# Kernel tuning notes

Measured on AMD Instinct MI355X. Metric: run time of the kernel, lower is better.

## Reference

```python
import jax, jax.numpy as jnp
import numpy as np

IN_FEATURES = 4096
OUT_FEATURES = 4096

def setup_inputs() -> dict:
    key = jax.random.key(0)
    kx, kw, kb = jax.random.split(key, 3)
    x = jax.random.normal(kx, (8192, IN_FEATURES), dtype=jnp.float32)
    weight = jax.random.normal(kw, (OUT_FEATURES, IN_FEATURES), dtype=jnp.float32)
    bias = jax.random.normal(kb, (OUT_FEATURES,), dtype=jnp.float32)
    return {"x": x, "weight": weight, "bias": bias}

def reference(x, weight, bias):
    # Binarize weights to {-1, 0, +1} via sign, then dense linear: y = x @ sign(W)^T + b
    w_bin = jnp.sign(weight)
    return jnp.einsum('bi,oi->bo', x, w_bin) + bias
```

## Files before the change

kernel.cpp:

```cpp
#include <hip/hip_runtime.h>
#include <hip/hip_bf16.h>
#include <stdint.h>

#define M_DIM 8192
#define N_DIM 4096
#define K_DIM 4096

#define NT 64

using i32x4 = __attribute__((ext_vector_type(4))) int;

typedef const __attribute__((address_space(1))) void glb_void_t;
typedef __attribute__((address_space(3))) void lds_void_t;

__device__ __forceinline__ void async16(const void* g, void* l) {
    __builtin_amdgcn_global_load_lds((glb_void_t*)(uintptr_t)g,
                                     (lds_void_t*)(uint32_t)(uintptr_t)l,
                                     16, 0, 0);
}

__device__ __forceinline__ int sgn_i8(float f) {
    union { float f; uint32_t u; } v; v.f = f;
    if ((v.u & 0x7FFFFFFFu) == 0u) return 0;
    return (v.u >> 31) ? -1 : 1;
}


__global__ void convert_w_kernel(const float* __restrict__ w,
                                 unsigned char* __restrict__ wq, int n4) {
    int stride = gridDim.x * blockDim.x;
    for (int i = blockIdx.x * blockDim.x + threadIdx.x; i < n4; i += stride) {
        float4 v = ((const float4*)w)[i];
        uint32_t o = ((uint32_t)(uint8_t)sgn_i8(v.x)) |
                     ((uint32_t)(uint8_t)sgn_i8(v.y) << 8) |
                     ((uint32_t)(uint8_t)sgn_i8(v.z) << 16) |
                     ((uint32_t)(uint8_t)sgn_i8(v.w) << 24);
        ((uint32_t*)wq)[i] = o;
    }
}


__global__ __launch_bounds__(256)
void convert_x_kernel(const float* __restrict__ x,
                      unsigned char* __restrict__ xq,
                      float* __restrict__ scales) {
    const int row = blockIdx.x;
    const int tid = threadIdx.x;
    const float4* xr = (const float4*)(x + (size_t)row * K_DIM);
    float4 v[4];
    float m = 0.f;
    #pragma unroll
    for (int j = 0; j < 4; ++j) {
        v[j] = xr[j * 256 + tid];
        m = fmaxf(m, fmaxf(fmaxf(fabsf(v[j].x), fabsf(v[j].y)),
                           fmaxf(fabsf(v[j].z), fabsf(v[j].w))));
    }
    #pragma unroll
    for (int off = 32; off >= 1; off >>= 1)
        m = fmaxf(m, __shfl_xor(m, off));
    __shared__ float wmax[4];
    if ((tid & 63) == 0) wmax[tid >> 6] = m;
    __syncthreads();
    m = fmaxf(fmaxf(wmax[0], wmax[1]), fmaxf(wmax[2], wmax[3]));
    const float inv = (m > 0.f) ? 127.0f / m : 0.f;
    if (tid == 0) scales[row] = (m > 0.f) ? m / 127.0f : 0.f;
    uint32_t* oq = (uint32_t*)(xq + (size_t)row * K_DIM);
    #pragma unroll
    for (int j = 0; j < 4; ++j) {
        float q0 = fminf(fmaxf(rintf(v[j].x * inv), -127.f), 127.f);
        float q1 = fminf(fmaxf(rintf(v[j].y * inv), -127.f), 127.f);
        float q2 = fminf(fmaxf(rintf(v[j].z * inv), -127.f), 127.f);
        float q3 = fminf(fmaxf(rintf(v[j].w * inv), -127.f), 127.f);
        uint32_t o = ((uint32_t)(uint8_t)(int)q0) |
                     ((uint32_t)(uint8_t)(int)q1 << 8) |
                     ((uint32_t)(uint8_t)(int)q2 << 16) |
                     ((uint32_t)(uint8_t)(int)q3 << 24);
        oq[j * 256 + tid] = o;
    }
}


#define BAR   __builtin_amdgcn_s_barrier()
#define VM2   asm volatile("s_waitcnt vmcnt(2)" ::: "memory")
#define VM0   asm volatile("s_waitcnt vmcnt(0)" ::: "memory")

#define RDA(BUFV, MLO) \
    _Pragma("unroll") for (int mm = 0; mm < 4; ++mm) \
        a[mm] = rdfrag((BUFV), wm, ((MLO) + mm) * 16);

#define RDB(BUFV) \
    _Pragma("unroll") for (int nn = 0; nn < 4; ++nn) \
        b[nn] = rdfrag((BUFV), sectB, rB + nn * 16);

#define MM16(MB) \
    __builtin_amdgcn_s_setprio(1); \
    _Pragma("unroll") for (int mm = 0; mm < 4; ++mm) \
    _Pragma("unroll") for (int nn = 0; nn < 4; ++nn) \
        acc[(MB) + mm][nn] = __builtin_amdgcn_mfma_i32_16x16x64_i8( \
            a[mm], b[nn], acc[(MB) + mm][nn], 0, 0, 0); \
    __builtin_amdgcn_s_setprio(0);

#define KT(T, SA, SB, VMW) do { \
    const int buf_ = (T) & 1; const int nbuf_ = buf_ ^ 1; \
    if (SA) stage(nbuf_, 0, xq, brow, ((T) + 1) * 64); \
    RDB(buf_) RDA(buf_, 0) \
    MM16(0) \
    if (SA) stage(nbuf_, 1, xq, brow + 128, ((T) + 1) * 64); \
    RDA(buf_, 4) \
    MM16(4) \
    BAR;                              \
    if (SB) stage(buf_, 2, wq, bcol, ((T) + 2) * 64); \
    if (SB) stage(buf_, 3, wq, bcol + 128, ((T) + 2) * 64); \
    VMW; \
    BAR;                              \
} while (0)

__global__ __launch_bounds__(512, 2)
void gemm_bin_kernel(const unsigned char* __restrict__ xq,
                     const unsigned char* __restrict__ wq,
                     const float* __restrict__ scales,
                     const float* __restrict__ bias,
                     float* __restrict__ out) {
    __shared__ __align__(16) unsigned char lds[2][4][8192];

    const int tid  = threadIdx.x;
    const int wid  = tid >> 6;
    const int lane = tid & 63;

    const int bid  = blockIdx.x;
    const int swzb = (bid & 7) * 64 + (bid >> 3);
    const int brow = (swzb >> 4) * 256;
    const int bcol = (swzb & 15) * 256;

    const int wm = wid >> 2;
    const int wn = wid & 3;
    const int fr  = lane & 15;
    const int g16 = (lane >> 4) << 4;
    const int sw  = ((lane >> 1) & 3) << 4;
    const int sectB = 2 + (wn >> 1);
    const int rB    = (wn & 1) * 64;

    i32x4 acc[8][4] = {};
    i32x4 a[4], b[4];

    const int srow = tid >> 2;
    const int scol = ((tid & 3) ^ ((tid >> 3) & 3)) * 16;
    auto stage = [&](int bufv, int sect, const unsigned char* g, int row0, int k0) {
        async16(g + (size_t)(row0 + srow) * K_DIM + (k0 + scol),
                &lds[bufv][sect][0] + tid * 16);
    };

    auto rdfrag = [&](int bufv, int sect, int rbase) -> i32x4 {
        const unsigned char* base = &lds[bufv][sect][0];
        return *(const i32x4*)(base + (rbase + fr) * 64 + (g16 ^ sw));
    };

    stage(0, 0, xq, brow,        0);
    stage(0, 1, xq, brow + 128,  0);
    stage(0, 2, wq, bcol,        0);
    stage(0, 3, wq, bcol + 128,  0);
    stage(1, 2, wq, bcol,       64);
    stage(1, 3, wq, bcol + 128, 64);
    VM2;
    BAR;

    #pragma unroll 2
    for (int t = 0; t < NT - 2; ++t) KT(t, 1, 1, VM2);
    KT(NT - 2, 1, 0, VM0);
    KT(NT - 1, 0, 0, (void)0);

    const int wrow = wm * 128, wcol = wn * 64;
    float bv[4];
    #pragma unroll
    for (int n = 0; n < 4; ++n) bv[n] = bias[bcol + wcol + n * 16 + fr];
    const int r4 = (lane >> 4) * 4;
    #pragma unroll
    for (int m = 0; m < 8; ++m) {
        #pragma unroll
        for (int rr = 0; rr < 4; ++rr) {
            const int row = brow + wrow + m * 16 + r4 + rr;
            const float sc = scales[row];
            float* orow = out + (size_t)row * N_DIM + bcol + wcol;
            #pragma unroll
            for (int n = 0; n < 4; ++n)
                orow[n * 16 + fr] = (float)acc[m][n][rr] * sc + bv[n];
        }
    }
}


__global__ void naive_kernel(const float* __restrict__ x,
                             const float* __restrict__ w,
                             const float* __restrict__ bias,
                             float* __restrict__ out) {
    const size_t total = (size_t)M_DIM * N_DIM;
    for (size_t idx = (size_t)blockIdx.x * blockDim.x + threadIdx.x; idx < total;
         idx += (size_t)gridDim.x * blockDim.x) {
        const size_t row = idx >> 12;
        const size_t col = idx & 4095;
        const float4* xr  = (const float4*)(x + row * K_DIM);
        const float4* wrp = (const float4*)(w + col * K_DIM);
        float s = 0.f;
        for (int k = 0; k < K_DIM / 4; ++k) {
            float4 a = xr[k], bq = wrp[k];
            s += a.x * (bq.x > 0.f ? 1.f : (bq.x < 0.f ? -1.f : 0.f));
            s += a.y * (bq.y > 0.f ? 1.f : (bq.y < 0.f ? -1.f : 0.f));
            s += a.z * (bq.z > 0.f ? 1.f : (bq.z < 0.f ? -1.f : 0.f));
            s += a.w * (bq.w > 0.f ? 1.f : (bq.w < 0.f ? -1.f : 0.f));
        }
        out[idx] = s + bias[col];
    }
}

extern "C" void kernel_launch(void* const* d_in, const int* in_sizes, int n_in,
                              void* d_out, int out_size, void* d_ws, size_t ws_size,
                              hipStream_t stream) {
    const float* x    = (const float*)d_in[0];
    const float* w    = (const float*)d_in[1];
    const float* bias = (const float*)d_in[2];
    float* out = (float*)d_out;

    const size_t xq_bytes = (size_t)M_DIM * K_DIM;
    const size_t wq_bytes = (size_t)N_DIM * K_DIM;
    const size_t sc_bytes = (size_t)M_DIM * sizeof(float);

    if (ws_size >= xq_bytes + wq_bytes + sc_bytes) {
        unsigned char* xq = (unsigned char*)d_ws;
        unsigned char* wq = (unsigned char*)d_ws + xq_bytes;
        float* scales     = (float*)((char*)d_ws + xq_bytes + wq_bytes);
        convert_w_kernel<<<2048, 256, 0, stream>>>(w, wq,
            (int)((size_t)N_DIM * K_DIM / 4));
        convert_x_kernel<<<M_DIM, 256, 0, stream>>>(x, xq, scales);
        gemm_bin_kernel<<<dim3((M_DIM / 256) * (N_DIM / 256)), dim3(512), 0, stream>>>(
            xq, wq, scales, bias, out);
    } else {
        naive_kernel<<<4096, 256, 0, stream>>>(x, w, bias, out);
    }
}
```

Measured before the change: 189.5 us.

## Switch int8 GEMM mainloop to triple-buffered LDS with one barrier per tile

The int8 MFMA GEMM main loop moves from a double-buffered LDS scheme, with split A/B staging and two barriers per k-tile, to a three-stage ring. All four sections of tile T+2 are issued at the top of each iteration, and a single vmcnt(4) wait plus one barrier follows. The aim is to prefetch further ahead and halve barrier synchronisation. LDS per block grows from 64 KB to 96 KB, which likely prevents the two blocks per CU requested by the launch bounds and lowers occupancy. The loop is no longer unrolled, so buffer indices are computed with a runtime modulo.

After: 187.1 us. No clear change (-1.2%).

```diff
diff --git a/kernel.cpp b/kernel.cpp
--- a/kernel.cpp
+++ b/kernel.cpp
@@ -81,7 +81,7 @@
 
 
 #define BAR   __builtin_amdgcn_s_barrier()
-#define VM2   asm volatile("s_waitcnt vmcnt(2)" ::: "memory")
+#define VM4   asm volatile("s_waitcnt vmcnt(4)" ::: "memory")
 #define VM0   asm volatile("s_waitcnt vmcnt(0)" ::: "memory")
 
 #define RDA(BUFV, MLO) \
@@ -100,19 +100,20 @@
             a[mm], b[nn], acc[(MB) + mm][nn], 0, 0, 0); \
     __builtin_amdgcn_s_setprio(0);
 
-#define KT(T, SA, SB, VMW) do { \
-    const int buf_ = (T) & 1; const int nbuf_ = buf_ ^ 1; \
-    if (SA) stage(nbuf_, 0, xq, brow, ((T) + 1) * 64); \
-    RDB(buf_) RDA(buf_, 0) \
+#define KT(T, S, VMW) do { \
+    const int cb_ = (T) % 3; const int pb_ = ((T) + 2) % 3; \
+    if (S) { \
+        stage(pb_, 0, xq, brow,       ((T) + 2) * 64); \
+        stage(pb_, 1, xq, brow + 128, ((T) + 2) * 64); \
+        stage(pb_, 2, wq, bcol,       ((T) + 2) * 64); \
+        stage(pb_, 3, wq, bcol + 128, ((T) + 2) * 64); \
+    } \
+    RDB(cb_) RDA(cb_, 0) \
     MM16(0) \
-    if (SA) stage(nbuf_, 1, xq, brow + 128, ((T) + 1) * 64); \
-    RDA(buf_, 4) \
+    RDA(cb_, 4) \
     MM16(4) \
-    BAR;                              \
-    if (SB) stage(buf_, 2, wq, bcol, ((T) + 2) * 64); \
-    if (SB) stage(buf_, 3, wq, bcol + 128, ((T) + 2) * 64); \
     VMW; \
-    BAR;                              \
+    BAR; \
 } while (0)
 
 __global__ __launch_bounds__(512, 2)
@@ -121,7 +122,7 @@
                      const float* __restrict__ scales,
                      const float* __restrict__ bias,
                      float* __restrict__ out) {
-    __shared__ __align__(16) unsigned char lds[2][4][8192];
+    __shared__ __align__(16) unsigned char lds[3][4][8192];
 
     const int tid  = threadIdx.x;
     const int wid  = tid >> 6;
@@ -159,15 +160,16 @@
     stage(0, 1, xq, brow + 128,  0);
     stage(0, 2, wq, bcol,        0);
     stage(0, 3, wq, bcol + 128,  0);
+    stage(1, 0, xq, brow,       64);
+    stage(1, 1, xq, brow + 128, 64);
     stage(1, 2, wq, bcol,       64);
     stage(1, 3, wq, bcol + 128, 64);
-    VM2;
+    VM4;
     BAR;
 
-    #pragma unroll 2
-    for (int t = 0; t < NT - 2; ++t) KT(t, 1, 1, VM2);
-    KT(NT - 2, 1, 0, VM0);
-    KT(NT - 1, 0, 0, (void)0);
+    for (int t = 0; t < NT - 2; ++t) KT(t, 1, VM4);
+    KT(NT - 2, 0, VM0);
+    KT(NT - 1, 0, (void)0);
 
     const int wrow = wm * 128, wcol = wn * 64;
     float bv[4];
```
